# Performance work log

Hardware: AMD Instinct MI355X
Metric: run time of the kernel (lower is better)

The kernel has to match this reference:

```python
import jax, jax.numpy as jnp
import numpy as np

N, E, B, K = 100000, 3200000, 500, 30
F_IN, H1, NUM_CLASSES = 128, 64, 18


def _gcn_conv(x, W, b, row, col, w_edge, n_nodes):
    # PyG GCNConv: remove_self_loops happened outside (w_edge=0 on self loops),
    # GCNConv re-adds self loops -> deg = in_deg + 1, norm = d^-1/2[row]*d^-1/2[col].
    xw = x @ W
    deg = jax.ops.segment_sum(w_edge, col, num_segments=n_nodes) + 1.0
    dis = jax.lax.rsqrt(deg)
    coef = dis[row] * dis[col] * w_edge           # [E]
    msg = xw[row] * coef[:, None]                 # [E, C] irregular gather
    agg = jax.ops.segment_sum(msg, col, num_segments=n_nodes)
    agg = agg + xw * (dis * dis)[:, None]         # self-loop term
    return agg + b


def _sort_pool(x, batch, num_graphs, k):
    # SortAggregation: per-graph sort descending by last channel, keep top-k, zero-pad.
    n, c = x.shape
    score = x[:, -1]
    perm = jnp.lexsort((-score, batch))           # sort by (batch asc, score desc)
    b_sorted = batch[perm]
    counts = jax.ops.segment_sum(jnp.ones((n,), x.dtype), batch, num_segments=num_graphs)
    starts = jnp.cumsum(counts) - counts          # segment start offsets
    pos = jnp.arange(n) - starts[b_sorted].astype(jnp.int32)
    pos = jnp.where(pos < k, pos, k)              # out-of-range -> dropped
    out = jnp.zeros((num_graphs, k, c), x.dtype).at[b_sorted, pos].set(x[perm], mode='drop')
    return out.reshape(num_graphs, k * c)


def _conv1d(x, w, b, stride):
    y = jax.lax.conv_general_dilated(x, w, (stride,), 'VALID',
                                     dimension_numbers=('NCH', 'OIH', 'NCH'))
    return y + b[None, :, None]


def setup_inputs() -> dict:
    key = jax.random.key(0)
    ks = jax.random.split(key, 16)
    x = jax.random.normal(ks[0], (N, F_IN), dtype=jnp.float32)
    edge_index = jax.random.randint(ks[1], (2, E), 0, N, dtype=jnp.int32)
    batch = jnp.sort(jax.random.randint(ks[2], (N,), 0, B, dtype=jnp.int32))
    s = 0.05
    return {
        'x': x, 'edge_index': edge_index, 'batch': batch, 'num_graphs': B,
        'W1': jax.random.normal(ks[3], (F_IN, H1), jnp.float32) * s,
        'b1': jnp.zeros((H1,), jnp.float32),
        'W2': jax.random.normal(ks[4], (H1, 1), jnp.float32) * s,
        'b2': jnp.zeros((1,), jnp.float32),
        'conv3_w': jax.random.normal(ks[5], (16, 1, 97), jnp.float32) * s,
        'conv3_b': jnp.zeros((16,), jnp.float32),
        'conv4_w': jax.random.normal(ks[6], (32, 16, 5), jnp.float32) * s,
        'conv4_b': jnp.zeros((32,), jnp.float32),
        'fc1_w': jax.random.normal(ks[7], (192, 128), jnp.float32) * s,
        'fc1_b': jnp.zeros((128,), jnp.float32),
        'fc2_w': jax.random.normal(ks[8], (128, NUM_CLASSES), jnp.float32) * s,
        'fc2_b': jnp.zeros((NUM_CLASSES,), jnp.float32),
    }


def reference(x, edge_index, batch, num_graphs, W1, b1, W2, b2,
              conv3_w, conv3_b, conv4_w, conv4_b, fc1_w, fc1_b, fc2_w, fc2_b):
    row, col = edge_index[0], edge_index[1]
    w_edge = (row != col).astype(x.dtype)         # remove_self_loops
    x1 = jnp.tanh(_gcn_conv(x, W1, b1, row, col, w_edge, x.shape[0]))   # [N,64]
    x2 = jnp.tanh(_gcn_conv(x1, W2, b2, row, col, w_edge, x.shape[0]))  # [N,1]
    xc = jnp.concatenate([x1, x2], axis=-1)       # [N,65]
    p = _sort_pool(xc, batch, num_graphs, K)      # [B, 1950]
    h = p[:, None, :]                             # [B,1,1950]
    h = jax.nn.relu(_conv1d(h, conv3_w, conv3_b, 97))                   # [B,16,20]
    h = jax.lax.reduce_window(h, -jnp.inf, jax.lax.max,
                              (1, 1, 2), (1, 1, 2), 'VALID')            # [B,16,10]
    h = jax.nn.relu(_conv1d(h, conv4_w, conv4_b, 1))                    # [B,32,6]
    h = h.reshape(h.shape[0], -1)                 # [B,192]
    last_layer = jax.nn.relu(h @ fc1_w + fc1_b)   # [B,128] (dropout = eval identity)
    out = last_layer @ fc2_w + fc2_b              # [B,18]
    classes = jax.nn.log_softmax(out, axis=-1)
    return (classes, out, last_layer)
```

## Files before the change

### kernel.cpp

```cpp
#include <hip/hip_runtime.h>
#include <math.h>

#define N_NODES 100000
#define N_EDGES 3200000
#define B_GRAPHS 500
#define K_TOP 30
#define F_INN 128
#define H1C 64
#define NUM_CLASSES 18
#define XC 65
#define P_LEN (K_TOP * XC)
#define C3_OUT 16
#define C3_K 97
#define C3_L 20
#define P2_L 10
#define C4_OUT 32
#define C4_K 5
#define C4_L 6
#define FC1_IN 192
#define FC1_OUT 128

#define BK_SHIFT 7
#define BK_NODES 128
#define NBKT ((N_NODES + BK_NODES - 1) / BK_NODES)
#define BSTRIDE 5120
#define MS_EPT 16
#define MS_EPB (256 * MS_EPT)

typedef __attribute__((ext_vector_type(8))) short bf16x8;
typedef __attribute__((ext_vector_type(4))) float f32x4;

static __device__ __forceinline__ unsigned short f2bf(float f) {
    unsigned int u = __float_as_uint(f);
    u += 0x7FFFu + ((u >> 16) & 1u);
    return (unsigned short)(u >> 16);
}
static __device__ __forceinline__ float bfl(unsigned int u) {
    return __uint_as_float(u << 16);
}
static __device__ __forceinline__ float bfh(unsigned int u) {
    return __uint_as_float(u & 0xFFFF0000u);
}

__global__ __launch_bounds__(256) void k_mscatter(const int* __restrict__ row,
                                                  const int* __restrict__ col,
                                                  int* __restrict__ gcur,
                                                  unsigned int* __restrict__ ebkt) {
    __shared__ int hist[NBKT];
    __shared__ int base[NBKT];
    int tid = threadIdx.x;
    for (int i = tid; i < NBKT; i += 256) hist[i] = 0;
    __syncthreads();
    unsigned int pk[MS_EPT];
    unsigned int pay[MS_EPT];
    int e0 = blockIdx.x * MS_EPB;
#pragma unroll
    for (int j = 0; j < MS_EPT; ++j) {
        int e = e0 + j * 256 + tid;
        pk[j] = 0xFFFFFFFFu;
        if (e < N_EDGES) {
            int r = row[e], c = col[e];
            if (r != c) {
                int b = c >> BK_SHIFT;
                int rank = atomicAdd(&hist[b], 1);
                pk[j] = ((unsigned int)b << 12) | (unsigned int)rank;
                pay[j] = ((unsigned int)r << BK_SHIFT) | (unsigned int)(c & (BK_NODES - 1));
            }
        }
    }
    __syncthreads();
    for (int i = tid; i < NBKT; i += 256)
        base[i] = hist[i] ? (i * BSTRIDE + atomicAdd(&gcur[i], hist[i])) : 0;
    __syncthreads();
#pragma unroll
    for (int j = 0; j < MS_EPT; ++j) {
        if (pk[j] != 0xFFFFFFFFu) {
            int b = pk[j] >> 12;
            int rank = pk[j] & 0xFFF;
            ebkt[base[b] + rank] = pay[j];
        }
    }
}

__global__ __launch_bounds__(256) void k_csr(const unsigned int* __restrict__ ebkt,
                                             const int* __restrict__ gcur,
                                             float* __restrict__ dis,
                                             int2* __restrict__ rowse,
                                             int* __restrict__ erow) {
    __shared__ int cnt[BK_NODES];
    __shared__ int s[256];
    __shared__ int cur[BK_NODES];
    int b = blockIdx.x, t = threadIdx.x;
    if (t < BK_NODES) cnt[t] = 0;
    __syncthreads();
    int lo = b * BSTRIDE;
    int hi = lo + gcur[b];
    for (int i = lo + t; i < hi; i += 256)
        atomicAdd(&cnt[ebkt[i] & (BK_NODES - 1)], 1);
    __syncthreads();
    int v = (t < BK_NODES) ? cnt[t] : 0;
    s[t] = v;
    __syncthreads();
    for (int off = 1; off < BK_NODES; off <<= 1) {
        int add = (t >= off) ? s[t - off] : 0;
        __syncthreads();
        s[t] += add;
        __syncthreads();
    }
    int ex = s[t] - v;
    if (t < BK_NODES) {
        int node = b * BK_NODES + t;
        if (node < N_NODES) {
            dis[node] = rsqrtf((float)v + 1.0f);
            rowse[node] = make_int2(lo + ex, lo + ex + v);
        }
        cur[t] = lo + ex;
    }
    __syncthreads();
    for (int i = lo + t; i < hi; i += 256) {
        unsigned int pk = ebkt[i];
        int cl = pk & (BK_NODES - 1);
        int slot = atomicAdd(&cur[cl], 1);
        erow[slot] = (int)((pk >> BK_SHIFT) << 7);
    }
}

__global__ __launch_bounds__(256) void k_xw1(const float* __restrict__ x,
                                             const float* __restrict__ W1,
                                             const float* __restrict__ dis,
                                             unsigned short* __restrict__ xw) {
    __shared__ unsigned short w1s[16 * 64 * 8];
    int tid = threadIdx.x;
    if (blockIdx.x == 0 && tid < 32)
        ((unsigned int*)(xw + (size_t)N_NODES * H1C))[tid] = 0;
    for (int idx = tid; idx < 16 * 64 * 8; idx += 256) {
        int f = idx >> 9;
        int l = (idx >> 3) & 63;
        int j = idx & 7;
        int kq = f >> 2, t4 = f & 3;
        int k = kq * 32 + ((l >> 4) << 3) + j;
        int n = t4 * 16 + (l & 15);
        w1s[idx] = f2bf(W1[k * H1C + n]);
    }
    __syncthreads();
    int wave = tid >> 6;
    int lane = tid & 63;
    int quad = lane >> 4;
    int m = lane & 15;
    int wrow0 = blockIdx.x * 64 + wave * 16;

    bf16x8 bw[16];
#pragma unroll
    for (int f = 0; f < 16; ++f)
        bw[f] = *(const bf16x8*)&w1s[(f * 64 + lane) * 8];

    f32x4 acc[4];
#pragma unroll
    for (int t = 0; t < 4; ++t) acc[t] = (f32x4){0.f, 0.f, 0.f, 0.f};

    int rowA = wrow0 + m;
    size_t ra = (size_t)(rowA < N_NODES ? rowA : N_NODES - 1);
#pragma unroll
    for (int kq = 0; kq < 4; ++kq) {
        const float* xp = x + ra * F_INN + kq * 32 + quad * 8;
        float4 f0 = ((const float4*)xp)[0];
        float4 f1 = ((const float4*)xp)[1];
        bf16x8 a;
        a[0] = (short)f2bf(f0.x); a[1] = (short)f2bf(f0.y);
        a[2] = (short)f2bf(f0.z); a[3] = (short)f2bf(f0.w);
        a[4] = (short)f2bf(f1.x); a[5] = (short)f2bf(f1.y);
        a[6] = (short)f2bf(f1.z); a[7] = (short)f2bf(f1.w);
#pragma unroll
        for (int t = 0; t < 4; ++t)
            acc[t] = __builtin_amdgcn_mfma_f32_16x16x32_bf16(a, bw[kq * 4 + t], acc[t], 0, 0, 0);
    }
#pragma unroll
    for (int r = 0; r < 4; ++r) {
        int rowD = wrow0 + quad * 4 + r;
        if (rowD < N_NODES) {
            float dsc = dis[rowD];
#pragma unroll
            for (int t = 0; t < 4; ++t)
                xw[(size_t)rowD * H1C + t * 16 + m] = f2bf(acc[t][r] * dsc);
        }
    }
}

__global__ __launch_bounds__(256) void k_agg1f(const int2* __restrict__ rowse,
                                               const int* __restrict__ erow,
                                               const unsigned short* __restrict__ xws,
                                               const float* __restrict__ dis,
                                               const float* __restrict__ b1,
                                               const float* __restrict__ W2,
                                               float* __restrict__ x1,
                                               float* __restrict__ xws2) {
    int wid = blockIdx.x * 4 + (threadIdx.x >> 6);
    int lane = threadIdx.x & 63;
    if (wid >= N_NODES) return;
    int grp = lane >> 3;
    int sub = lane & 7;
    int2 se = rowse[wid];
    int base = se.x, endp = se.y;
    const char* xb = (const char*)xws;
    const int ZR = N_NODES << 7;
    float acc[8] = {0.f, 0.f, 0.f, 0.f, 0.f, 0.f, 0.f, 0.f};
    for (int e0 = base; e0 < endp; e0 += 16) {
        int i0 = e0 + grp;
        int i1 = e0 + 8 + grp;
        int o0 = (i0 < endp) ? erow[i0] : ZR;
        int o1 = (i1 < endp) ? erow[i1] : ZR;
        uint4 a = ((const uint4*)(xb + o0))[sub];
        uint4 bq = ((const uint4*)(xb + o1))[sub];
        acc[0] += bfl(a.x) + bfl(bq.x);
        acc[1] += bfh(a.x) + bfh(bq.x);
        acc[2] += bfl(a.y) + bfl(bq.y);
        acc[3] += bfh(a.y) + bfh(bq.y);
        acc[4] += bfl(a.z) + bfl(bq.z);
        acc[5] += bfh(a.z) + bfh(bq.z);
        acc[6] += bfl(a.w) + bfl(bq.w);
        acc[7] += bfh(a.w) + bfh(bq.w);
    }
#pragma unroll
    for (int i = 0; i < 8; ++i) {
        acc[i] += __shfl_xor(acc[i], 8);
        acc[i] += __shfl_xor(acc[i], 16);
        acc[i] += __shfl_xor(acc[i], 32);
    }
    if (grp == 0) {
        float d = dis[wid];
        uint4 ow = ((const uint4*)(xb + ((size_t)wid << 7)))[sub];
        float self[8] = {bfl(ow.x), bfh(ow.x), bfl(ow.y), bfh(ow.y),
                         bfl(ow.z), bfh(ow.z), bfl(ow.w), bfh(ow.w)};
        float4 bb0 = ((const float4*)b1)[sub * 2];
        float4 bb1 = ((const float4*)b1)[sub * 2 + 1];
        float r[8];
        r[0] = tanhf(d * (acc[0] + self[0]) + bb0.x);
        r[1] = tanhf(d * (acc[1] + self[1]) + bb0.y);
        r[2] = tanhf(d * (acc[2] + self[2]) + bb0.z);
        r[3] = tanhf(d * (acc[3] + self[3]) + bb0.w);
        r[4] = tanhf(d * (acc[4] + self[4]) + bb1.x);
        r[5] = tanhf(d * (acc[5] + self[5]) + bb1.y);
        r[6] = tanhf(d * (acc[6] + self[6]) + bb1.z);
        r[7] = tanhf(d * (acc[7] + self[7]) + bb1.w);
        ((float4*)(x1 + (size_t)wid * H1C))[sub * 2] = make_float4(r[0], r[1], r[2], r[3]);
        ((float4*)(x1 + (size_t)wid * H1C))[sub * 2 + 1] = make_float4(r[4], r[5], r[6], r[7]);
        float4 w20 = ((const float4*)W2)[sub * 2];
        float4 w21 = ((const float4*)W2)[sub * 2 + 1];
        float s = r[0] * w20.x + r[1] * w20.y + r[2] * w20.z + r[3] * w20.w +
                  r[4] * w21.x + r[5] * w21.y + r[6] * w21.z + r[7] * w21.w;
        s += __shfl_xor(s, 1);
        s += __shfl_xor(s, 2);
        s += __shfl_xor(s, 4);
        if (sub == 0) xws2[wid] = d * s;
    }
}

__global__ __launch_bounds__(256) void k_poolhead(const int* __restrict__ batch,
                                                  const float* __restrict__ x1,
                                                  const int2* __restrict__ rowse,
                                                  const int* __restrict__ erow,
                                                  const float* __restrict__ xws2,
                                                  const float* __restrict__ dis,
                                                  const float* __restrict__ b2,
                                                  const float* __restrict__ w3, const float* __restrict__ b3,
                                                  const float* __restrict__ w4, const float* __restrict__ b4,
                                                  const float* __restrict__ fw1, const float* __restrict__ fb1,
                                                  const float* __restrict__ fw2, const float* __restrict__ fb2,
                                                  float* __restrict__ out) {
    __shared__ float x2s[512];
    __shared__ int sel[K_TOP];
    __shared__ float ps[P_LEN];
    __shared__ float h1s[C3_OUT * C3_L];
    __shared__ float h2s[C3_OUT * P2_L];
    __shared__ float h3s[FC1_IN];
    __shared__ float lls[FC1_OUT];
    __shared__ float outs[NUM_CLASSES];
    int g = blockIdx.x, tid = threadIdx.x;
    int lo = 0, hi = N_NODES;
    while (lo < hi) { int m = (lo + hi) >> 1; if (batch[m] < g) lo = m + 1; else hi = m; }
    int start = lo;
    hi = N_NODES;
    while (lo < hi) { int m = (lo + hi) >> 1; if (batch[m] < g + 1) lo = m + 1; else hi = m; }
    int end = lo;
    int count = end - start;
    if (count > 512) count = 512;
    float b2v = b2[0];
    for (int t = tid; t < count; t += 256) {
        int node = start + t;
        int2 se = rowse[node];
        float acc = 0.0f;
        for (int idx = se.x; idx < se.y; ++idx)
            acc += xws2[erow[idx] >> 7];
        x2s[t] = tanhf(dis[node] * (acc + xws2[node]) + b2v);
    }
    __syncthreads();
    int wave = tid >> 6, lane = tid & 63;
    if (wave == 0) {
        unsigned long long k[8];
#pragma unroll
        for (int i = 0; i < 8; ++i) {
            int idx = i * 64 + lane;
            unsigned long long key = 0ULL;
            if (idx < count) {
                unsigned int bits = __float_as_uint(x2s[idx]);
                unsigned int u = (bits & 0x80000000u) ? ~bits : (bits | 0x80000000u);
                key = ((unsigned long long)u << 32) | (unsigned int)(~(unsigned int)(start + idx));
            }
            k[i] = key;
        }
        int kk = count < K_TOP ? count : K_TOP;
        for (int j = 0; j < kk; ++j) {
            unsigned long long best = k[0];
#pragma unroll
            for (int i = 1; i < 8; ++i) if (k[i] > best) best = k[i];
#pragma unroll
            for (int off = 32; off; off >>= 1) {
                unsigned long long o = __shfl_xor(best, off);
                if (o > best) best = o;
            }
            int node = (int)(~(unsigned int)(best & 0xFFFFFFFFULL));
#pragma unroll
            for (int i = 0; i < 8; ++i) if (k[i] == best) k[i] = 0ULL;
            if (lane == 0) sel[j] = node;
        }
        if (lane >= kk && lane < K_TOP) sel[lane] = -1;
    }
    __syncthreads();
    for (int t = tid; t < P_LEN; t += 256) {
        int j = t / XC, c = t - j * XC;
        int node = sel[j];
        float v = 0.0f;
        if (node >= 0) v = (c < H1C) ? x1[(size_t)node * H1C + c] : x2s[node - start];
        ps[t] = v;
    }
    __syncthreads();
    for (int o = tid; o < C3_OUT * C3_L; o += 256) {
        int oc = o / C3_L, pos = o % C3_L;
        float s = b3[oc];
        const float* w = w3 + oc * C3_K;
        int base = pos * C3_K;
        for (int k = 0; k < C3_K; ++k) s += ps[base + k] * w[k];
        h1s[o] = fmaxf(s, 0.0f);
    }
    __syncthreads();
    if (tid < C3_OUT * P2_L) {
        int oc = tid / P2_L, pos = tid % P2_L;
        h2s[tid] = fmaxf(h1s[oc * C3_L + 2 * pos], h1s[oc * C3_L + 2 * pos + 1]);
    }
    __syncthreads();
    if (tid < C4_OUT * C4_L) {
        int oc = tid / C4_L, pos = tid % C4_L;
        float s = b4[oc];
        for (int ic = 0; ic < C3_OUT; ++ic)
#pragma unroll
            for (int k = 0; k < C4_K; ++k)
                s += h2s[ic * P2_L + pos + k] * w4[oc * C3_OUT * C4_K + ic * C4_K + k];
        h3s[oc * C4_L + pos] = fmaxf(s, 0.0f);
    }
    __syncthreads();
    if (tid < FC1_OUT) {
        float s = fb1[tid];
        for (int i = 0; i < FC1_IN; ++i) s += h3s[i] * fw1[i * FC1_OUT + tid];
        float v = fmaxf(s, 0.0f);
        lls[tid] = v;
        out[2 * B_GRAPHS * NUM_CLASSES + (size_t)g * FC1_OUT + tid] = v;
    }
    __syncthreads();
    if (tid < NUM_CLASSES) {
        float s = fb2[tid];
        for (int j = 0; j < FC1_OUT; ++j) s += lls[j] * fw2[j * NUM_CLASSES + tid];
        outs[tid] = s;
        out[B_GRAPHS * NUM_CLASSES + (size_t)g * NUM_CLASSES + tid] = s;
    }
    __syncthreads();
    if (tid < NUM_CLASSES) {
        float m = -INFINITY;
        for (int k2 = 0; k2 < NUM_CLASSES; ++k2) m = fmaxf(m, outs[k2]);
        float se = 0.0f;
        for (int k2 = 0; k2 < NUM_CLASSES; ++k2) se += expf(outs[k2] - m);
        out[(size_t)g * NUM_CLASSES + tid] = outs[tid] - m - logf(se);
    }
}

extern "C" void kernel_launch(void* const* d_in, const int* in_sizes, int n_in,
                              void* d_out, int out_size, void* d_ws, size_t ws_size,
                              hipStream_t stream) {
    const float* x   = (const float*)d_in[0];
    const int*   ei  = (const int*)d_in[1];
    const int*   row = ei;
    const int*   col = ei + N_EDGES;
    const int*   bat = (const int*)d_in[2];
    const float* W1  = (const float*)d_in[4];
    const float* b1  = (const float*)d_in[5];
    const float* W2  = (const float*)d_in[6];
    const float* b2  = (const float*)d_in[7];
    const float* w3  = (const float*)d_in[8];
    const float* b3  = (const float*)d_in[9];
    const float* w4  = (const float*)d_in[10];
    const float* b4  = (const float*)d_in[11];
    const float* fw1 = (const float*)d_in[12];
    const float* fb1 = (const float*)d_in[13];
    const float* fw2 = (const float*)d_in[14];
    const float* fb2 = (const float*)d_in[15];

    char* wsb = (char*)d_ws;
    unsigned short* xws = (unsigned short*)wsb;       wsb += (size_t)(N_NODES + 1) * H1C * 2;
    float* x1     = (float*)wsb;                      wsb += (size_t)N_NODES * H1C * 4;
    int*   erow   = (int*)wsb;                        wsb += (size_t)NBKT * BSTRIDE * 4;
    unsigned int* ebkt = (unsigned int*)x1;
    int*   gcur   = (int*)wsb;                        wsb += (size_t)NBKT * 4;
    int2*  rowse  = (int2*)wsb;                       wsb += (size_t)N_NODES * 8;
    float* dis    = (float*)wsb;                      wsb += (size_t)N_NODES * 4;
    float* xws2   = (float*)wsb;                      wsb += (size_t)N_NODES * 4;
    float* outp   = (float*)d_out;

    hipMemsetAsync(gcur, 0, (size_t)NBKT * 4, stream);

    k_mscatter<<<(N_EDGES + MS_EPB - 1) / MS_EPB, 256, 0, stream>>>(row, col, gcur, ebkt);
    k_csr<<<NBKT, 256, 0, stream>>>(ebkt, gcur, dis, rowse, erow);
    k_xw1<<<(N_NODES + 63) / 64, 256, 0, stream>>>(x, W1, dis, xws);
    k_agg1f<<<(N_NODES + 3) / 4, 256, 0, stream>>>(rowse, erow, xws, dis, b1, W2, x1, xws2);
    k_poolhead<<<B_GRAPHS, 256, 0, stream>>>(bat, x1, rowse, erow, xws2, dis, b2,
                                             w3, b3, w4, b4, fw1, fb1, fw2, fb2, outp);
}
```

Baseline: 339.4 us.

## Split layer-2 aggregation into its own grid-wide kernel and spread k_agg1f epilogue

The second GCN layer's per-node aggregation moves out of the per-graph pooling kernel into a new kernel, k_x2. In k_x2 each node is handled by 8 lanes in parallel, instead of one thread per node serially walking its edges inside only 500 blocks. The k_agg1f epilogue now stages reduced accumulators in shared memory so all 64 lanes compute tanh and the W2 dot product, rather than only 8 lanes doing 8 each. The aim is better parallelism and load balance for the serial edge loops in k_poolhead. The cost is an extra launch, an x2 buffer round trip, and a __syncthreads. The bounds checks are also removed, which relies on N being divisible by 4 and by 32.

```diff
diff --git a/kernel.cpp b/kernel.cpp
--- a/kernel.cpp
+++ b/kernel.cpp
@@ -194,9 +194,11 @@
                                                const float* __restrict__ W2,
                                                float* __restrict__ x1,
                                                float* __restrict__ xws2) {
-    int wid = blockIdx.x * 4 + (threadIdx.x >> 6);
-    int lane = threadIdx.x & 63;
-    if (wid >= N_NODES) return;
+    __shared__ float accs[4][64];
+    int tid = threadIdx.x;
+    int wave = tid >> 6;
+    int lane = tid & 63;
+    int wid = blockIdx.x * 4 + wave;
     int grp = lane >> 3;
     int sub = lane & 7;
     int2 se = rowse[wid];
@@ -227,41 +229,46 @@
         acc[i] += __shfl_xor(acc[i], 32);
     }
     if (grp == 0) {
-        float d = dis[wid];
-        uint4 ow = ((const uint4*)(xb + ((size_t)wid << 7)))[sub];
-        float self[8] = {bfl(ow.x), bfh(ow.x), bfl(ow.y), bfh(ow.y),
-                         bfl(ow.z), bfh(ow.z), bfl(ow.w), bfh(ow.w)};
-        float4 bb0 = ((const float4*)b1)[sub * 2];
-        float4 bb1 = ((const float4*)b1)[sub * 2 + 1];
-        float r[8];
-        r[0] = tanhf(d * (acc[0] + self[0]) + bb0.x);
-        r[1] = tanhf(d * (acc[1] + self[1]) + bb0.y);
-        r[2] = tanhf(d * (acc[2] + self[2]) + bb0.z);
-        r[3] = tanhf(d * (acc[3] + self[3]) + bb0.w);
-        r[4] = tanhf(d * (acc[4] + self[4]) + bb1.x);
-        r[5] = tanhf(d * (acc[5] + self[5]) + bb1.y);
-        r[6] = tanhf(d * (acc[6] + self[6]) + bb1.z);
-        r[7] = tanhf(d * (acc[7] + self[7]) + bb1.w);
-        ((float4*)(x1 + (size_t)wid * H1C))[sub * 2] = make_float4(r[0], r[1], r[2], r[3]);
-        ((float4*)(x1 + (size_t)wid * H1C))[sub * 2 + 1] = make_float4(r[4], r[5], r[6], r[7]);
-        float4 w20 = ((const float4*)W2)[sub * 2];
-        float4 w21 = ((const float4*)W2)[sub * 2 + 1];
-        float s = r[0] * w20.x + r[1] * w20.y + r[2] * w20.z + r[3] * w20.w +
-                  r[4] * w21.x + r[5] * w21.y + r[6] * w21.z + r[7] * w21.w;
-        s += __shfl_xor(s, 1);
-        s += __shfl_xor(s, 2);
-        s += __shfl_xor(s, 4);
-        if (sub == 0) xws2[wid] = d * s;
-    }
+#pragma unroll
+        for (int i = 0; i < 8; ++i) accs[wave][sub * 8 + i] = acc[i];
+    }
+    __syncthreads();
+    float d = dis[wid];
+    unsigned int su = xws[(size_t)wid * H1C + lane];
+    float self = __uint_as_float(su << 16);
+    float v = tanhf(d * (accs[wave][lane] + self) + b1[lane]);
+    x1[(size_t)wid * H1C + lane] = v;
+    float s = v * W2[lane];
+#pragma unroll
+    for (int off = 1; off < 64; off <<= 1) s += __shfl_xor(s, off);
+    if (lane == 0) xws2[wid] = d * s;
+}
+
+__global__ __launch_bounds__(256) void k_x2(const int2* __restrict__ rowse,
+                                            const int* __restrict__ erow,
+                                            const float* __restrict__ xws2,
+                                            const float* __restrict__ dis,
+                                            const float* __restrict__ b2,
+                                            float* __restrict__ x2) {
+    int lane = threadIdx.x & 63;
+    int wglob = (blockIdx.x * 256 + threadIdx.x) >> 6;
+    int grp = lane >> 3;
+    int sub = lane & 7;
+    int node = wglob * 8 + grp;
+    int2 se = rowse[node];
+    float acc = 0.0f;
+    for (int i = se.x + sub; i < se.y; i += 8)
+        acc += xws2[erow[i] >> 7];
+    acc += __shfl_xor(acc, 1);
+    acc += __shfl_xor(acc, 2);
+    acc += __shfl_xor(acc, 4);
+    if (sub == 0)
+        x2[node] = tanhf(dis[node] * (acc + xws2[node]) + b2[0]);
 }
 
 __global__ __launch_bounds__(256) void k_poolhead(const int* __restrict__ batch,
                                                   const float* __restrict__ x1,
-                                                  const int2* __restrict__ rowse,
-                                                  const int* __restrict__ erow,
-                                                  const float* __restrict__ xws2,
-                                                  const float* __restrict__ dis,
-                                                  const float* __restrict__ b2,
+                                                  const float* __restrict__ x2,
                                                   const float* __restrict__ w3, const float* __restrict__ b3,
                                                   const float* __restrict__ w4, const float* __restrict__ b4,
                                                   const float* __restrict__ fw1, const float* __restrict__ fb1,
@@ -284,15 +291,7 @@
     int end = lo;
     int count = end - start;
     if (count > 512) count = 512;
-    float b2v = b2[0];
-    for (int t = tid; t < count; t += 256) {
-        int node = start + t;
-        int2 se = rowse[node];
-        float acc = 0.0f;
-        for (int idx = se.x; idx < se.y; ++idx)
-            acc += xws2[erow[idx] >> 7];
-        x2s[t] = tanhf(dis[node] * (acc + xws2[node]) + b2v);
-    }
+    for (int t = tid; t < count; t += 256) x2s[t] = x2[start + t];
     __syncthreads();
     int wave = tid >> 6, lane = tid & 63;
     if (wave == 0) {
@@ -412,6 +411,7 @@
     int2*  rowse  = (int2*)wsb;                       wsb += (size_t)N_NODES * 8;
     float* dis    = (float*)wsb;                      wsb += (size_t)N_NODES * 4;
     float* xws2   = (float*)wsb;                      wsb += (size_t)N_NODES * 4;
+    float* x2     = (float*)wsb;                      wsb += (size_t)N_NODES * 4;
     float* outp   = (float*)d_out;
 
     hipMemsetAsync(gcur, 0, (size_t)NBKT * 4, stream);
@@ -419,7 +419,8 @@
     k_mscatter<<<(N_EDGES + MS_EPB - 1) / MS_EPB, 256, 0, stream>>>(row, col, gcur, ebkt);
     k_csr<<<NBKT, 256, 0, stream>>>(ebkt, gcur, dis, rowse, erow);
     k_xw1<<<(N_NODES + 63) / 64, 256, 0, stream>>>(x, W1, dis, xws);
-    k_agg1f<<<(N_NODES + 3) / 4, 256, 0, stream>>>(rowse, erow, xws, dis, b1, W2, x1, xws2);
-    k_poolhead<<<B_GRAPHS, 256, 0, stream>>>(bat, x1, rowse, erow, xws2, dis, b2,
+    k_agg1f<<<N_NODES / 4, 256, 0, stream>>>(rowse, erow, xws, dis, b1, W2, x1, xws2);
+    k_x2<<<N_NODES / (8 * 4), 256, 0, stream>>>(rowse, erow, xws2, dis, b2, x2);
+    k_poolhead<<<B_GRAPHS, 256, 0, stream>>>(bat, x1, x2,
                                              w3, b3, w4, b4, fw1, fb1, fw2, fb2, outp);
 }
```

New measurement: 334.8 us. About the same (-1.4%).
